# Kernel tuning notes

Hardware: AMD Instinct MI355X
Metric: run time of the kernel (lower is better)

The kernel has to match this reference:

```python
import jax, jax.numpy as jnp
import numpy as np

B, S, D, H = 2, 2048, 1024, 16
DK = D // H


def setup_inputs() -> dict:
    key = jax.random.key(0)
    ks = jax.random.split(key, 11)
    std = 1.0 / np.sqrt(D)
    inp = {
        "query": jax.random.normal(ks[0], (B, S, D), jnp.float32),
        "key": jax.random.normal(ks[1], (B, S, D), jnp.float32),
        "value": jax.random.normal(ks[2], (B, S, D), jnp.float32),
        # True = masked position (torch masked_fill semantics); causal mask
        "mask": jnp.triu(jnp.ones((1, 1, S, S), jnp.bool_), k=1),
        "Wq": jax.random.normal(ks[3], (D, D), jnp.float32) * std,
        "bq": jnp.zeros((D,), jnp.float32),
        "Wk": jax.random.normal(ks[4], (D, D), jnp.float32) * std,
        "bk": jnp.zeros((D,), jnp.float32),
        "Wv": jax.random.normal(ks[5], (D, D), jnp.float32) * std,
        "bv": jnp.zeros((D,), jnp.float32),
        "Wo": jax.random.normal(ks[6], (D, D), jnp.float32) * std,
        "bo": jnp.zeros((D,), jnp.float32),
    }
    return inp


def _split_heads(x):
    b, s, _ = x.shape
    return x.reshape(b, s, H, DK).transpose(0, 2, 1, 3)  # [b, H, s, dk]


def reference(query, key, value, mask, Wq, bq, Wk, bk, Wv, bv, Wo, bo):
    q = _split_heads(query @ Wq + bq)
    k = _split_heads(key @ Wk + bk)
    v = _split_heads(value @ Wv + bv)
    scale = 1.0 / (DK ** 0.5)
    logits = jnp.einsum("bhqd,bhkd->bhqk", q, k) * scale
    logits = jnp.where(mask, -1.0e9, logits)
    w = jax.nn.softmax(logits, axis=-1)
    att = jnp.einsum("bhqk,bhkd->bhqd", w, v)  # [B, H, S, dk]
    # NOTE: faithful to the original bug -- view() without permuting heads back,
    # i.e. a raw row-major reshape [B,H,S,dk] -> [B,S,H*dk].
    att = att.reshape(att.shape[0], att.shape[2], -1)
    out = att @ Wo + bo
    return out
```

## Files before the change

kernel.cpp:

```cpp
#include <hip/hip_runtime.h>
#include <hip/hip_bf16.h>

typedef __hip_bfloat16 bf16;
typedef __attribute__((ext_vector_type(8))) short bf16x8;
typedef __attribute__((ext_vector_type(4))) float f32x4;

constexpr int Bc  = 2;
constexpr int Sc  = 2048;
constexpr int Dc  = 1024;
constexpr int Hc  = 16;
constexpr int DKc = 64;

__device__ __forceinline__ float bfbits2f(unsigned short u) {
  return __uint_as_float(((unsigned)u) << 16);
}
__device__ __forceinline__ unsigned short f2bfbits(float x) {
  bf16 h = __float2bfloat16(x);
  return *reinterpret_cast<unsigned short*>(&h);
}
__device__ __forceinline__ void store1_dyn(char* base, size_t ei, int isf32, float v) {
  if (isf32) *reinterpret_cast<float*>(base + ei * 4) = v;
  else       *reinterpret_cast<bf16*>(base + ei * 2) = __float2bfloat16(v);
}
__device__ __forceinline__ float fast_exp2(float x) {
  return __builtin_amdgcn_exp2f(x);
}
__device__ __forceinline__ uint4 pack8(const float4& a, const float4& b) {
  uint4 r;
  r.x = (unsigned)f2bfbits(a.x) | ((unsigned)f2bfbits(a.y) << 16);
  r.y = (unsigned)f2bfbits(a.z) | ((unsigned)f2bfbits(a.w) << 16);
  r.z = (unsigned)f2bfbits(b.x) | ((unsigned)f2bfbits(b.y) << 16);
  r.w = (unsigned)f2bfbits(b.z) | ((unsigned)f2bfbits(b.w) << 16);
  return r;
}

__global__ void detect_dtype(const unsigned short* __restrict__ q, int* __restrict__ flag) {
  __shared__ int cnt[256];
  const int tid = threadIdx.x;
  int c = 0;
  for (int i = tid; i < 2048; i += 256) {
    const unsigned short u = q[i];
    const int e = (u >> 7) & 0xFF;
    if (e >= 134 || e <= 90) ++c;
  }
  cnt[tid] = c;
  __syncthreads();
  for (int s = 128; s > 0; s >>= 1) {
    if (tid < s) cnt[tid] += cnt[tid + s];
    __syncthreads();
  }
  if (tid == 0) flag[0] = (cnt[0] > 64) ? 1 : 0;
}

__global__ __launch_bounds__(256)
void transpose_w4(const char* __restrict__ W0, const char* __restrict__ W1,
                  const char* __restrict__ W2, const char* __restrict__ W3,
                  unsigned short* __restrict__ Wt_all, const int* __restrict__ flagp) {
  __shared__ unsigned short T[64][72];
  const int dyn = flagp[0];
  const int z = blockIdx.z;
  const char* W = (z == 0) ? W0 : (z == 1) ? W1 : (z == 2) ? W2 : W3;
  unsigned short* Wt = Wt_all + (size_t)z * Dc * Dc;
  const int tid = threadIdx.x;
  const int n0 = blockIdx.x * 64, k0 = blockIdx.y * 64;
  const int r = tid >> 2, c16 = (tid & 3) * 16;

  unsigned short us[16];
  if (dyn) {
    const float4* p = reinterpret_cast<const float4*>(
        W + ((size_t)(k0 + r) * Dc + n0 + c16) * 4);
    const float4 f0 = p[0], f1 = p[1], f2 = p[2], f3 = p[3];
    const float fv[16] = {f0.x, f0.y, f0.z, f0.w, f1.x, f1.y, f1.z, f1.w,
                          f2.x, f2.y, f2.z, f2.w, f3.x, f3.y, f3.z, f3.w};
#pragma unroll
    for (int i = 0; i < 16; ++i) us[i] = f2bfbits(fv[i]);
  } else {
    const ushort4* p = reinterpret_cast<const ushort4*>(
        W + ((size_t)(k0 + r) * Dc + n0 + c16) * 2);
    const ushort4 u0 = p[0], u1 = p[1], u2 = p[2], u3 = p[3];
    us[0] = u0.x;  us[1] = u0.y;  us[2] = u0.z;  us[3] = u0.w;
    us[4] = u1.x;  us[5] = u1.y;  us[6] = u1.z;  us[7] = u1.w;
    us[8] = u2.x;  us[9] = u2.y;  us[10] = u2.z; us[11] = u2.w;
    us[12] = u3.x; us[13] = u3.y; us[14] = u3.z; us[15] = u3.w;
  }
#pragma unroll
  for (int i = 0; i < 16; ++i) T[r][c16 + i] = us[i];
  __syncthreads();

  unsigned vs[8];
#pragma unroll
  for (int i = 0; i < 8; ++i)
    vs[i] = (unsigned)T[c16 + 2 * i][r] | ((unsigned)T[c16 + 2 * i + 1][r] << 16);
  uint4* op = reinterpret_cast<uint4*>(Wt + (size_t)(n0 + r) * Dc + k0 + c16);
  op[0] = make_uint4(vs[0], vs[1], vs[2], vs[3]);
  op[1] = make_uint4(vs[4], vs[5], vs[6], vs[7]);
}

__global__ void conv_bias(const char* __restrict__ b0, const char* __restrict__ b1,
                          const char* __restrict__ b2, const char* __restrict__ b3,
                          unsigned short* __restrict__ out, const int* __restrict__ flagp) {
  const int dyn = flagp[0];
  const char* src = (blockIdx.x == 0) ? b0 : (blockIdx.x == 1) ? b1
                    : (blockIdx.x == 2) ? b2 : b3;
  for (int i = threadIdx.x; i < Dc; i += 256) {
    float v = dyn ? reinterpret_cast<const float*>(src)[i]
                  : bfbits2f(reinterpret_cast<const unsigned short*>(src)[i]);
    out[blockIdx.x * Dc + i] = f2bfbits(v);
  }
}

__global__ __launch_bounds__(256)
void qkv_gemm(const char* __restrict__ A0, const char* __restrict__ A1,
              const char* __restrict__ A2, const unsigned short* __restrict__ Wt_all,
              const unsigned short* __restrict__ bias_all,
              bf16* __restrict__ C0, bf16* __restrict__ C1, bf16* __restrict__ C2,
              const int* __restrict__ flagp) {
  constexpr int K = Dc, N = Dc;
  __shared__ __align__(16) unsigned short At[128][32];
  __shared__ __align__(16) unsigned short Bt[128][32];

  const int z = blockIdx.z;
  const char* A = (z == 0) ? A0 : (z == 1) ? A1 : A2;
  bf16* C = (z == 0) ? C0 : (z == 1) ? C1 : C2;
  const float scale = (z == 0) ? 0.18033688011112042f : 1.0f;
  const unsigned short* Wt = Wt_all + (size_t)z * Dc * Dc;
  const unsigned short* bias = bias_all + z * Dc;
  const int af = flagp[0];

  const int tid = threadIdx.x;
  const int m0 = blockIdx.x * 128, n0 = blockIdx.y * 128;
  const int w = tid >> 6, lane = tid & 63;
  const int lo16 = lane & 15, quad = lane >> 4;
  const int wm = (w >> 1) * 64, wn = (w & 1) * 64;
  const int sr = tid >> 1, sh = (tid & 1) * 16;

  f32x4 acc[4][4] = {};

  for (int k0 = 0; k0 < K; k0 += 32) {
    uint4 a_lo, a_hi;
    if (af) {
      const float4* p = reinterpret_cast<const float4*>(
          A + ((size_t)(m0 + sr) * K + k0 + sh) * 4);
      a_lo = pack8(p[0], p[1]);
      a_hi = pack8(p[2], p[3]);
    } else {
      const uint4* p = reinterpret_cast<const uint4*>(
          A + ((size_t)(m0 + sr) * K + k0 + sh) * 2);
      a_lo = p[0];
      a_hi = p[1];
    }
    const uint4* wp = reinterpret_cast<const uint4*>(Wt + (size_t)(n0 + sr) * K + k0 + sh);
    const uint4 b_lo = wp[0], b_hi = wp[1];

    __syncthreads();
    *reinterpret_cast<uint4*>(&At[sr][sh])     = a_lo;
    *reinterpret_cast<uint4*>(&At[sr][sh + 8]) = a_hi;
    *reinterpret_cast<uint4*>(&Bt[sr][sh])     = b_lo;
    *reinterpret_cast<uint4*>(&Bt[sr][sh + 8]) = b_hi;
    __syncthreads();

    bf16x8 afr[4], bfr[4];
#pragma unroll
    for (int mt = 0; mt < 4; ++mt)
      afr[mt] = *reinterpret_cast<const bf16x8*>(&At[wm + mt * 16 + lo16][quad * 8]);
#pragma unroll
    for (int nt = 0; nt < 4; ++nt)
      bfr[nt] = *reinterpret_cast<const bf16x8*>(&Bt[wn + nt * 16 + lo16][quad * 8]);
#pragma unroll
    for (int mt = 0; mt < 4; ++mt)
#pragma unroll
      for (int nt = 0; nt < 4; ++nt)
        acc[mt][nt] = __builtin_amdgcn_mfma_f32_16x16x32_bf16(afr[mt], bfr[nt],
                                                              acc[mt][nt], 0, 0, 0);
  }

  float bv[4];
#pragma unroll
  for (int nt = 0; nt < 4; ++nt)
    bv[nt] = bfbits2f(bias[n0 + wn + nt * 16 + lo16]);
#pragma unroll
  for (int mt = 0; mt < 4; ++mt)
#pragma unroll
    for (int r = 0; r < 4; ++r) {
      const int row = m0 + wm + mt * 16 + quad * 4 + r;
#pragma unroll
      for (int nt = 0; nt < 4; ++nt) {
        const int col = n0 + wn + nt * 16 + lo16;
        C[(size_t)row * N + col] = __float2bfloat16((acc[mt][nt][r] + bv[nt]) * scale);
      }
    }
}

__global__ __launch_bounds__(256)
void out_gemm(const bf16* __restrict__ A, const unsigned short* __restrict__ Wt,
              const unsigned short* __restrict__ bias, char* __restrict__ C,
              const int* __restrict__ flagp) {
  constexpr int K = Dc, N = Dc;
  __shared__ __align__(16) unsigned short At[64][32];
  __shared__ __align__(16) unsigned short Bt[128][32];

  const int cf = flagp[0];
  const int tid = threadIdx.x;
  const int m0 = blockIdx.x * 64, n0 = blockIdx.y * 128;
  const int w = tid >> 6, lane = tid & 63;
  const int lo16 = lane & 15, quad = lane >> 4;
  const int wm = (w >> 1) * 32, wn = (w & 1) * 64;
  const int ar = tid >> 2, ah = (tid & 3) * 8;
  const int br = tid >> 1, bh = (tid & 1) * 16;

  f32x4 acc[2][4] = {};

  for (int k0 = 0; k0 < K; k0 += 32) {
    const uint4 a0 = *reinterpret_cast<const uint4*>(A + (size_t)(m0 + ar) * K + k0 + ah);
    const uint4* wp = reinterpret_cast<const uint4*>(Wt + (size_t)(n0 + br) * K + k0 + bh);
    const uint4 b_lo = wp[0], b_hi = wp[1];

    __syncthreads();
    *reinterpret_cast<uint4*>(&At[ar][ah])     = a0;
    *reinterpret_cast<uint4*>(&Bt[br][bh])     = b_lo;
    *reinterpret_cast<uint4*>(&Bt[br][bh + 8]) = b_hi;
    __syncthreads();

    bf16x8 afr[2], bfr[4];
#pragma unroll
    for (int mt = 0; mt < 2; ++mt)
      afr[mt] = *reinterpret_cast<const bf16x8*>(&At[wm + mt * 16 + lo16][quad * 8]);
#pragma unroll
    for (int nt = 0; nt < 4; ++nt)
      bfr[nt] = *reinterpret_cast<const bf16x8*>(&Bt[wn + nt * 16 + lo16][quad * 8]);
#pragma unroll
    for (int mt = 0; mt < 2; ++mt)
#pragma unroll
      for (int nt = 0; nt < 4; ++nt)
        acc[mt][nt] = __builtin_amdgcn_mfma_f32_16x16x32_bf16(afr[mt], bfr[nt],
                                                              acc[mt][nt], 0, 0, 0);
  }

  float bv[4];
#pragma unroll
  for (int nt = 0; nt < 4; ++nt)
    bv[nt] = bfbits2f(bias[n0 + wn + nt * 16 + lo16]);
#pragma unroll
  for (int mt = 0; mt < 2; ++mt)
#pragma unroll
    for (int r = 0; r < 4; ++r) {
      const int row = m0 + wm + mt * 16 + quad * 4 + r;
#pragma unroll
      for (int nt = 0; nt < 4; ++nt) {
        const int col = n0 + wn + nt * 16 + lo16;
        store1_dyn(C, (size_t)row * N + col, cf, acc[mt][nt][r] + bv[nt]);
      }
    }
}

__global__ __launch_bounds__(256)
void attn_mfma(const bf16* __restrict__ Q, const bf16* __restrict__ K,
               const bf16* __restrict__ V, bf16* __restrict__ O) {
  __shared__ __align__(16) unsigned short Kt[64][72];
  __shared__ __align__(16) unsigned short Vt[64][72];
  __shared__ __align__(16) unsigned short St[4][16][72];
  __shared__ float Li[4][16];

  const int b = blockIdx.z, h = blockIdx.y;
  const int tid = threadIdx.x;
  const int w = tid >> 6;
  const int lane = tid & 63;
  const int lo16 = lane & 15, quad = lane >> 4;
  const size_t hd = (size_t)h * DKc;

  const int kr = tid >> 2, kc = (tid & 3) * 16;
  const int vk = (tid & 31) * 2, vd0 = (tid >> 5) * 8;

  for (int pi = 0; pi < 2; ++pi) {
    const int qt = pi ? (31 - blockIdx.x) : blockIdx.x;
    const int q0 = qt * 64;

    const bf16* qrow = Q + ((size_t)(b * Sc + q0 + w * 16 + lo16)) * Dc + hd;
    const bf16x8 qa0 = *reinterpret_cast<const bf16x8*>(qrow + quad * 8);
    const bf16x8 qa1 = *reinterpret_cast<const bf16x8*>(qrow + 32 + quad * 8);

    f32x4 oacc[4] = {f32x4{0,0,0,0}, f32x4{0,0,0,0}, f32x4{0,0,0,0}, f32x4{0,0,0,0}};
    float lsum = 0.f;
    const int qg = q0 + w * 16 + lo16;

    for (int t = 0; t <= qt; ++t) {
      const int kt = t * 64;
      __syncthreads();
      {
        const bf16* kp = K + ((size_t)(b * Sc + kt + kr)) * Dc + hd + kc;
        const uint4 k0v = *reinterpret_cast<const uint4*>(kp);
        const uint4 k1v = *reinterpret_cast<const uint4*>(kp + 8);
        *reinterpret_cast<uint4*>(&Kt[kr][kc])     = k0v;
        *reinterpret_cast<uint4*>(&Kt[kr][kc + 8]) = k1v;
      }
      {
        const bf16* vbase = V + ((size_t)(b * Sc + kt + vk)) * Dc + hd + vd0;
        const uint4 ra = *reinterpret_cast<const uint4*>(vbase);
        const uint4 rb = *reinterpret_cast<const uint4*>(vbase + Dc);
        *reinterpret_cast<unsigned*>(&Vt[vd0 + 0][vk]) = (ra.x & 0xffffu) | (rb.x << 16);
        *reinterpret_cast<unsigned*>(&Vt[vd0 + 1][vk]) = (ra.x >> 16)     | (rb.x & 0xffff0000u);
        *reinterpret_cast<unsigned*>(&Vt[vd0 + 2][vk]) = (ra.y & 0xffffu) | (rb.y << 16);
        *reinterpret_cast<unsigned*>(&Vt[vd0 + 3][vk]) = (ra.y >> 16)     | (rb.y & 0xffff0000u);
        *reinterpret_cast<unsigned*>(&Vt[vd0 + 4][vk]) = (ra.z & 0xffffu) | (rb.z << 16);
        *reinterpret_cast<unsigned*>(&Vt[vd0 + 5][vk]) = (ra.z >> 16)     | (rb.z & 0xffff0000u);
        *reinterpret_cast<unsigned*>(&Vt[vd0 + 6][vk]) = (ra.w & 0xffffu) | (rb.w << 16);
        *reinterpret_cast<unsigned*>(&Vt[vd0 + 7][vk]) = (ra.w >> 16)     | (rb.w & 0xffff0000u);
      }
      __syncthreads();

      f32x4 s[4] = {f32x4{0,0,0,0}, f32x4{0,0,0,0}, f32x4{0,0,0,0}, f32x4{0,0,0,0}};
#pragma unroll
      for (int ct = 0; ct < 4; ++ct) {
        const bf16x8 ka0 = *reinterpret_cast<const bf16x8*>(&Kt[ct * 16 + lo16][quad * 8]);
        const bf16x8 ka1 = *reinterpret_cast<const bf16x8*>(&Kt[ct * 16 + lo16][32 + quad * 8]);
        s[ct] = __builtin_amdgcn_mfma_f32_16x16x32_bf16(ka0, qa0, s[ct], 0, 0, 0);
        s[ct] = __builtin_amdgcn_mfma_f32_16x16x32_bf16(ka1, qa1, s[ct], 0, 0, 0);
      }

      if (kt + 63 > q0 + w * 16) {
#pragma unroll
        for (int ct = 0; ct < 4; ++ct)
#pragma unroll
          for (int r = 0; r < 4; ++r)
            if (kt + ct * 16 + quad * 4 + r > qg) s[ct][r] = -1e9f;
      }

#pragma unroll
      for (int ct = 0; ct < 4; ++ct) {
        const float p0 = fast_exp2(fminf(s[ct][0], 43.f));
        const float p1 = fast_exp2(fminf(s[ct][1], 43.f));
        const float p2 = fast_exp2(fminf(s[ct][2], 43.f));
        const float p3 = fast_exp2(fminf(s[ct][3], 43.f));
        lsum += (p0 + p1) + (p2 + p3);
        uint2 pk;
        pk.x = (unsigned)f2bfbits(p0) | ((unsigned)f2bfbits(p1) << 16);
        pk.y = (unsigned)f2bfbits(p2) | ((unsigned)f2bfbits(p3) << 16);
        *reinterpret_cast<uint2*>(&St[w][lo16][ct * 16 + quad * 4]) = pk;
      }

      const bf16x8 pa0 = *reinterpret_cast<const bf16x8*>(&St[w][lo16][quad * 8]);
      const bf16x8 pa1 = *reinterpret_cast<const bf16x8*>(&St[w][lo16][32 + quad * 8]);
#pragma unroll
      for (int ct = 0; ct < 4; ++ct) {
        const bf16x8 vb0 = *reinterpret_cast<const bf16x8*>(&Vt[ct * 16 + lo16][quad * 8]);
        const bf16x8 vb1 = *reinterpret_cast<const bf16x8*>(&Vt[ct * 16 + lo16][32 + quad * 8]);
        oacc[ct] = __builtin_amdgcn_mfma_f32_16x16x32_bf16(pa0, vb0, oacc[ct], 0, 0, 0);
        oacc[ct] = __builtin_amdgcn_mfma_f32_16x16x32_bf16(pa1, vb1, oacc[ct], 0, 0, 0);
      }
    }

    lsum += __shfl_xor(lsum, 16);
    lsum += __shfl_xor(lsum, 32);
    if (quad == 0) Li[w][lo16] = 1.f / lsum;
    __builtin_amdgcn_wave_barrier();
    const f32x4 invv = *reinterpret_cast<const f32x4*>(&Li[w][quad * 4]);

#pragma unroll
    for (int r = 0; r < 4; ++r) {
      bf16* op = O + (((size_t)(b * Hc + h) * Sc) + q0 + w * 16 + quad * 4 + r) * DKc + lo16;
#pragma unroll
      for (int ct = 0; ct < 4; ++ct)
        op[ct * 16] = __float2bfloat16(oacc[ct][r] * invv[r]);
    }
  }
}

extern "C" void kernel_launch(void* const* d_in, const int* in_sizes, int n_in,
                              void* d_out, int out_size, void* d_ws, size_t ws_size,
                              hipStream_t stream) {
  (void)in_sizes; (void)out_size; (void)ws_size;
  const char* query = (const char*)d_in[0];
  const char* key_  = (const char*)d_in[1];
  const char* value = (const char*)d_in[2];
  const int wb = n_in - 8;
  const char* Wq = (const char*)d_in[wb + 0];
  const char* bq = (const char*)d_in[wb + 1];
  const char* Wk = (const char*)d_in[wb + 2];
  const char* bk = (const char*)d_in[wb + 3];
  const char* Wv = (const char*)d_in[wb + 4];
  const char* bv = (const char*)d_in[wb + 5];
  const char* Wo = (const char*)d_in[wb + 6];
  const char* bo = (const char*)d_in[wb + 7];

  char* ws = (char*)d_ws;
  bf16* Qs  = (bf16*)(ws);
  bf16* Ks  = (bf16*)(ws + ((size_t)8  << 20));
  bf16* Vs  = (bf16*)(ws + ((size_t)16 << 20));
  bf16* att = (bf16*)(ws + ((size_t)24 << 20));
  unsigned short* Wt_all = (unsigned short*)(ws + ((size_t)32 << 20));
  unsigned short* bb_all = (unsigned short*)(ws + ((size_t)40 << 20));
  int* flag = (int*)(ws + ((size_t)40 << 20) + 16384);

  detect_dtype<<<1, 256, 0, stream>>>((const unsigned short*)query, flag);

  transpose_w4<<<dim3(16, 16, 4), 256, 0, stream>>>(Wq, Wk, Wv, Wo, Wt_all, flag);
  conv_bias<<<4, 256, 0, stream>>>(bq, bk, bv, bo, bb_all, flag);

  qkv_gemm<<<dim3(32, 8, 3), 256, 0, stream>>>(query, key_, value, Wt_all, bb_all,
                                               Qs, Ks, Vs, flag);

  attn_mfma<<<dim3(16, Hc, Bc), 256, 0, stream>>>(Qs, Ks, Vs, att);

  out_gemm<<<dim3(64, 8), 256, 0, stream>>>(att, Wt_all + (size_t)3 * Dc * Dc,
                                            bb_all + 3 * Dc, (char*)d_out, flag);
}
```

Before: 267.1 us.

## Use direct global-to-LDS loads in GEMMs with a pre-converted bf16 input path

Adds a prep kernel that converts the fp32 query/key/value inputs to bf16 in workspace. When the workspace is large enough, a new QKV GEMM loads tiles with global_load_lds straight into shared memory. The output GEMM switches to the same async LDS loads, and the attention grid is flattened to 1D so head/batch vary fastest within a query tile. This trades an extra full pass over the inputs for simpler, register-free tile loading; the unpadded LDS layout may cause bank conflicts, and the loop has no double buffering.

```diff
diff --git a/kernel.cpp b/kernel.cpp
--- a/kernel.cpp
+++ b/kernel.cpp
@@ -32,6 +32,11 @@
   r.z = (unsigned)f2bfbits(b.x) | ((unsigned)f2bfbits(b.y) << 16);
   r.w = (unsigned)f2bfbits(b.z) | ((unsigned)f2bfbits(b.w) << 16);
   return r;
+}
+__device__ __forceinline__ void gld16(const void* g, void* l) {
+  __builtin_amdgcn_global_load_lds(
+      (const __attribute__((address_space(1))) unsigned int*)g,
+      (__attribute__((address_space(3))) unsigned int*)l, 16, 0, 0);
 }
 
 __global__ void detect_dtype(const unsigned short* __restrict__ q, int* __restrict__ flag) {
@@ -50,6 +55,29 @@
     __syncthreads();
   }
   if (tid == 0) flag[0] = (cnt[0] > 64) ? 1 : 0;
+}
+
+__global__ __launch_bounds__(256)
+void prep_convert(const char* __restrict__ A0, const char* __restrict__ A1,
+                  const char* __restrict__ A2, bf16* __restrict__ B0,
+                  bf16* __restrict__ B1, bf16* __restrict__ B2,
+                  const int* __restrict__ flagp) {
+  const int dyn = flagp[0];
+  const int z = blockIdx.y;
+  const char* src = (z == 0) ? A0 : (z == 1) ? A1 : A2;
+  bf16* dst = (z == 0) ? B0 : (z == 1) ? B1 : B2;
+  const size_t n = (size_t)4096 * Dc;
+  const size_t stride = (size_t)512 * 256 * 8;
+  for (size_t i = ((size_t)blockIdx.x * 256 + threadIdx.x) * 8; i < n; i += stride) {
+    uint4 u;
+    if (dyn) {
+      const float4* p = reinterpret_cast<const float4*>(src + i * 4);
+      u = pack8(p[0], p[1]);
+    } else {
+      u = *reinterpret_cast<const uint4*>(src + i * 2);
+    }
+    *reinterpret_cast<uint4*>(dst + i) = u;
+  }
 }
 
 __global__ __launch_bounds__(256)
@@ -110,6 +138,77 @@
 }
 
 __global__ __launch_bounds__(256)
+void qkv_gemm_async(const bf16* __restrict__ A0, const bf16* __restrict__ A1,
+                    const bf16* __restrict__ A2,
+                    const unsigned short* __restrict__ Wt_all,
+                    const unsigned short* __restrict__ bias_all,
+                    bf16* __restrict__ C0, bf16* __restrict__ C1,
+                    bf16* __restrict__ C2) {
+  constexpr int K = Dc, N = Dc;
+  __shared__ __align__(16) unsigned short At[128 * 32];
+  __shared__ __align__(16) unsigned short Bt[128 * 32];
+
+  const int z = blockIdx.z;
+  const bf16* A = (z == 0) ? A0 : (z == 1) ? A1 : A2;
+  bf16* C = (z == 0) ? C0 : (z == 1) ? C1 : C2;
+  const float scale = (z == 0) ? 0.18033688011112042f : 1.0f;
+  const unsigned short* Wt = Wt_all + (size_t)z * Dc * Dc;
+  const unsigned short* bias = bias_all + z * Dc;
+
+  const int tid = threadIdx.x;
+  const int m0 = blockIdx.x * 128, n0 = blockIdx.y * 128;
+  const int w = tid >> 6, lane = tid & 63;
+  const int lo16 = lane & 15, quad = lane >> 4;
+  const int wm = (w >> 1) * 64, wn = (w & 1) * 64;
+
+  unsigned short* ldsA = &At[w * 1024 + lane * 8];
+  unsigned short* ldsB = &Bt[w * 1024 + lane * 8];
+  const bf16* gA = A + (size_t)(m0 + w * 32 + (lane >> 2)) * K + (lane & 3) * 8;
+  const unsigned short* gB = Wt + (size_t)(n0 + w * 32 + (lane >> 2)) * K + (lane & 3) * 8;
+
+  f32x4 acc[4][4] = {};
+
+  for (int k0 = 0; k0 < K; k0 += 32) {
+    gld16(gA + k0, ldsA);
+    gld16(gA + (size_t)16 * K + k0, ldsA + 512);
+    gld16(gB + k0, ldsB);
+    gld16(gB + (size_t)16 * K + k0, ldsB + 512);
+    __syncthreads();
+
+    bf16x8 afr[4], bfr[4];
+#pragma unroll
+    for (int mt = 0; mt < 4; ++mt)
+      afr[mt] = *reinterpret_cast<const bf16x8*>(&At[(wm + mt * 16 + lo16) * 32 + quad * 8]);
+#pragma unroll
+    for (int nt = 0; nt < 4; ++nt)
+      bfr[nt] = *reinterpret_cast<const bf16x8*>(&Bt[(wn + nt * 16 + lo16) * 32 + quad * 8]);
+#pragma unroll
+    for (int mt = 0; mt < 4; ++mt)
+#pragma unroll
+      for (int nt = 0; nt < 4; ++nt)
+        acc[mt][nt] = __builtin_amdgcn_mfma_f32_16x16x32_bf16(afr[mt], bfr[nt],
+                                                              acc[mt][nt], 0, 0, 0);
+    __syncthreads();
+  }
+
+  float bv[4];
+#pragma unroll
+  for (int nt = 0; nt < 4; ++nt)
+    bv[nt] = bfbits2f(bias[n0 + wn + nt * 16 + lo16]);
+#pragma unroll
+  for (int mt = 0; mt < 4; ++mt)
+#pragma unroll
+    for (int r = 0; r < 4; ++r) {
+      const int row = m0 + wm + mt * 16 + quad * 4 + r;
+#pragma unroll
+      for (int nt = 0; nt < 4; ++nt) {
+        const int col = n0 + wn + nt * 16 + lo16;
+        C[(size_t)row * N + col] = __float2bfloat16((acc[mt][nt][r] + bv[nt]) * scale);
+      }
+    }
+}
+
+__global__ __launch_bounds__(256)
 void qkv_gemm(const char* __restrict__ A0, const char* __restrict__ A1,
               const char* __restrict__ A2, const unsigned short* __restrict__ Wt_all,
               const unsigned short* __restrict__ bias_all,
@@ -192,12 +291,12 @@
 }
 
 __global__ __launch_bounds__(256)
-void out_gemm(const bf16* __restrict__ A, const unsigned short* __restrict__ Wt,
-              const unsigned short* __restrict__ bias, char* __restrict__ C,
-              const int* __restrict__ flagp) {
+void out_gemm_async(const bf16* __restrict__ A, const unsigned short* __restrict__ Wt,
+                    const unsigned short* __restrict__ bias, char* __restrict__ C,
+                    const int* __restrict__ flagp) {
   constexpr int K = Dc, N = Dc;
-  __shared__ __align__(16) unsigned short At[64][32];
-  __shared__ __align__(16) unsigned short Bt[128][32];
+  __shared__ __align__(16) unsigned short At[64 * 32];
+  __shared__ __align__(16) unsigned short Bt[128 * 32];
 
   const int cf = flagp[0];
   const int tid = threadIdx.x;
@@ -205,35 +304,34 @@
   const int w = tid >> 6, lane = tid & 63;
   const int lo16 = lane & 15, quad = lane >> 4;
   const int wm = (w >> 1) * 32, wn = (w & 1) * 64;
-  const int ar = tid >> 2, ah = (tid & 3) * 8;
-  const int br = tid >> 1, bh = (tid & 1) * 16;
+
+  unsigned short* ldsA = &At[w * 512 + lane * 8];
+  unsigned short* ldsB = &Bt[w * 1024 + lane * 8];
+  const bf16* gA = A + (size_t)(m0 + w * 16 + (lane >> 2)) * K + (lane & 3) * 8;
+  const unsigned short* gB = Wt + (size_t)(n0 + w * 32 + (lane >> 2)) * K + (lane & 3) * 8;
 
   f32x4 acc[2][4] = {};
 
   for (int k0 = 0; k0 < K; k0 += 32) {
-    const uint4 a0 = *reinterpret_cast<const uint4*>(A + (size_t)(m0 + ar) * K + k0 + ah);
-    const uint4* wp = reinterpret_cast<const uint4*>(Wt + (size_t)(n0 + br) * K + k0 + bh);
-    const uint4 b_lo = wp[0], b_hi = wp[1];
-
-    __syncthreads();
-    *reinterpret_cast<uint4*>(&At[ar][ah])     = a0;
-    *reinterpret_cast<uint4*>(&Bt[br][bh])     = b_lo;
-    *reinterpret_cast<uint4*>(&Bt[br][bh + 8]) = b_hi;
+    gld16(gA + k0, ldsA);
+    gld16(gB + k0, ldsB);
+    gld16(gB + (size_t)16 * K + k0, ldsB + 512);
     __syncthreads();
 
     bf16x8 afr[2], bfr[4];
 #pragma unroll
     for (int mt = 0; mt < 2; ++mt)
-      afr[mt] = *reinterpret_cast<const bf16x8*>(&At[wm + mt * 16 + lo16][quad * 8]);
+      afr[mt] = *reinterpret_cast<const bf16x8*>(&At[(wm + mt * 16 + lo16) * 32 + quad * 8]);
 #pragma unroll
     for (int nt = 0; nt < 4; ++nt)
-      bfr[nt] = *reinterpret_cast<const bf16x8*>(&Bt[wn + nt * 16 + lo16][quad * 8]);
+      bfr[nt] = *reinterpret_cast<const bf16x8*>(&Bt[(wn + nt * 16 + lo16) * 32 + quad * 8]);
 #pragma unroll
     for (int mt = 0; mt < 2; ++mt)
 #pragma unroll
       for (int nt = 0; nt < 4; ++nt)
         acc[mt][nt] = __builtin_amdgcn_mfma_f32_16x16x32_bf16(afr[mt], bfr[nt],
                                                               acc[mt][nt], 0, 0, 0);
+    __syncthreads();
   }
 
   float bv[4];
@@ -261,7 +359,9 @@
   __shared__ __align__(16) unsigned short St[4][16][72];
   __shared__ float Li[4][16];
 
-  const int b = blockIdx.z, h = blockIdx.y;
+  const int hb = blockIdx.x & 31;
+  const int bx = blockIdx.x >> 5;
+  const int b = hb >> 4, h = hb & 15;
   const int tid = threadIdx.x;
   const int w = tid >> 6;
   const int lane = tid & 63;
@@ -272,7 +372,7 @@
   const int vk = (tid & 31) * 2, vd0 = (tid >> 5) * 8;
 
   for (int pi = 0; pi < 2; ++pi) {
-    const int qt = pi ? (31 - blockIdx.x) : blockIdx.x;
+    const int qt = pi ? (31 - bx) : bx;
     const int q0 = qt * 64;
 
     const bf16* qrow = Q + ((size_t)(b * Sc + q0 + w * 16 + lo16)) * Dc + hd;
@@ -368,7 +468,7 @@
 extern "C" void kernel_launch(void* const* d_in, const int* in_sizes, int n_in,
                               void* d_out, int out_size, void* d_ws, size_t ws_size,
                               hipStream_t stream) {
-  (void)in_sizes; (void)out_size; (void)ws_size;
+  (void)in_sizes; (void)out_size;
   const char* query = (const char*)d_in[0];
   const char* key_  = (const char*)d_in[1];
   const char* value = (const char*)d_in[2];
@@ -390,17 +490,27 @@
   unsigned short* Wt_all = (unsigned short*)(ws + ((size_t)32 << 20));
   unsigned short* bb_all = (unsigned short*)(ws + ((size_t)40 << 20));
   int* flag = (int*)(ws + ((size_t)40 << 20) + 16384);
+  bf16* Qb = (bf16*)(ws + ((size_t)42 << 20));
+  bf16* Kb = (bf16*)(ws + ((size_t)50 << 20));
+  bf16* Vb = (bf16*)(ws + ((size_t)58 << 20));
+  const bool big_ws = ws_size >= ((size_t)66 << 20);
 
   detect_dtype<<<1, 256, 0, stream>>>((const unsigned short*)query, flag);
 
   transpose_w4<<<dim3(16, 16, 4), 256, 0, stream>>>(Wq, Wk, Wv, Wo, Wt_all, flag);
   conv_bias<<<4, 256, 0, stream>>>(bq, bk, bv, bo, bb_all, flag);
 
-  qkv_gemm<<<dim3(32, 8, 3), 256, 0, stream>>>(query, key_, value, Wt_all, bb_all,
-                                               Qs, Ks, Vs, flag);
-
-  attn_mfma<<<dim3(16, Hc, Bc), 256, 0, stream>>>(Qs, Ks, Vs, att);
-
-  out_gemm<<<dim3(64, 8), 256, 0, stream>>>(att, Wt_all + (size_t)3 * Dc * Dc,
-                                            bb_all + 3 * Dc, (char*)d_out, flag);
-}
+  if (big_ws) {
+    prep_convert<<<dim3(512, 3), 256, 0, stream>>>(query, key_, value, Qb, Kb, Vb, flag);
+    qkv_gemm_async<<<dim3(32, 8, 3), 256, 0, stream>>>(Qb, Kb, Vb, Wt_all, bb_all,
+                                                       Qs, Ks, Vs);
+  } else {
+    qkv_gemm<<<dim3(32, 8, 3), 256, 0, stream>>>(query, key_, value, Wt_all, bb_all,
+                                                 Qs, Ks, Vs, flag);
+  }
+
+  attn_mfma<<<dim3(512), 256, 0, stream>>>(Qs, Ks, Vs, att);
+
+  out_gemm_async<<<dim3(64, 8), 256, 0, stream>>>(att, Wt_all + (size_t)3 * Dc * Dc,
+                                                  bb_all + 3 * Dc, (char*)d_out, flag);
+}
```

Result: faster. 241.7 us (-9.5%).
